# Kernel tuning notes

Measured on AMD Instinct MI355X. Metric: run time of the kernel, lower is better.

## Reference

```python
import jax, jax.numpy as jnp
import numpy as np

HEADS = 8
DIM_HEAD = 64
SCALE = DIM_HEAD ** -0.5


def setup_inputs() -> dict:
    key = jax.random.key(0)
    k1, k2, k3 = jax.random.split(key, 3)
    B, N, D = 4, 2048, HEADS * DIM_HEAD  # D = inner_dim = 512
    x = jax.random.normal(k1, (B, N, D), dtype=jnp.float32)
    # nn.Linear weights stored transposed vs torch; here we use [in, out]
    w_qkv = jax.random.normal(k2, (D, 3 * D), dtype=jnp.float32) * (D ** -0.5)
    w_out = jax.random.normal(k3, (D, D), dtype=jnp.float32) * (D ** -0.5)
    b_out = jnp.zeros((D,), dtype=jnp.float32)
    return {"x": x, "w_qkv": w_qkv, "w_out": w_out, "b_out": b_out}


def reference(x, w_qkv, w_out, b_out):
    B, N, D = x.shape
    qkv = x @ w_qkv  # [B, N, 3D]
    q, k, v = jnp.split(qkv, 3, axis=-1)

    def to_heads(t):  # b n (h d) -> b h n d
        return t.reshape(B, N, HEADS, DIM_HEAD).transpose(0, 2, 1, 3)

    q, k, v = to_heads(q), to_heads(k), to_heads(v)
    dots = jnp.einsum('bhnd,bhmd->bhnm', q, k) * SCALE  # [B,H,N,N]
    attn = jax.nn.softmax(dots, axis=-1)
    out = jnp.einsum('bhnm,bhmd->bhnd', attn, v)  # [B,H,N,d]
    out = out.transpose(0, 2, 1, 3).reshape(B, N, D)  # b h n d -> b n (h d)
    return out @ w_out + b_out
```

## Files before the change

### kernel.cpp

```cpp
#include <hip/hip_runtime.h>

typedef __bf16 bf16;
typedef __bf16 bf16x8 __attribute__((ext_vector_type(8)));
typedef __bf16 bf16x4 __attribute__((ext_vector_type(4)));
typedef float f32x4 __attribute__((ext_vector_type(4)));
typedef float f32x16 __attribute__((ext_vector_type(16)));

#define MFMA16(a, b, c) __builtin_amdgcn_mfma_f32_16x16x32_bf16(a, b, c, 0, 0, 0)
#define MFMA32(a, b, c) __builtin_amdgcn_mfma_f32_32x32x16_bf16(a, b, c, 0, 0, 0)

#define CS 0.18033688011112042f

#if __has_builtin(__builtin_amdgcn_exp2f)
#define EXP2(x) __builtin_amdgcn_exp2f(x)
#else
#define EXP2(x) exp2f(x)
#endif

#define WAIT_VM0() __builtin_amdgcn_s_waitcnt(0x0F70)

__device__ __forceinline__ void load_lds16(const bf16* g, bf16* l) {
    __builtin_amdgcn_global_load_lds(
        (const __attribute__((address_space(1))) unsigned int*)g,
        (__attribute__((address_space(3))) unsigned int*)l, 16, 0, 0);
}

__device__ __forceinline__ bf16x4 shfl_xor32_b64(bf16x4 v) {
    union { bf16x4 b; int i[2]; } u;
    u.b = v;
    u.i[0] = __shfl_xor(u.i[0], 32, 64);
    u.i[1] = __shfl_xor(u.i[1], 32, 64);
    return u.b;
}

__device__ __forceinline__ bf16x8 build_bfrag(bf16x4 plo, bf16x4 phi, int h) {
    bf16x4 xlo = shfl_xor32_b64(plo);
    bf16x4 xhi = shfl_xor32_b64(phi);
    bf16x4 lo4 = h ? xhi : plo;
    bf16x4 hi4 = h ? phi : xlo;
    bf16x8 bb;
#pragma unroll
    for (int i = 0; i < 4; ++i) { bb[i] = lo4[i]; bb[4 + i] = hi4[i]; }
    return bb;
}

__global__ __launch_bounds__(256) void f32_to_bf16_kernel(const float* __restrict__ in,
                                                          bf16* __restrict__ out, int n) {
    int i = (blockIdx.x * 256 + threadIdx.x) * 4;
    if (i < n) {
        float4 v = *(const float4*)&in[i];
        bf16x4 o = {(bf16)v.x, (bf16)v.y, (bf16)v.z, (bf16)v.w};
        *(bf16x4*)&out[i] = o;
    }
}

__global__ __launch_bounds__(256) void transpose_f2b(const float* __restrict__ in,
                                                     bf16* __restrict__ out,
                                                     int R, int C) {
    __shared__ float tile[32][33];
    int tx = threadIdx.x & 31, ty = threadIdx.x >> 5;
    int c0 = blockIdx.x * 32, r0 = blockIdx.y * 32;
#pragma unroll
    for (int i = ty; i < 32; i += 8)
        tile[i][tx] = in[(size_t)(r0 + i) * C + c0 + tx];
    __syncthreads();
#pragma unroll
    for (int i = ty; i < 32; i += 8)
        out[(size_t)(c0 + i) * R + r0 + tx] = (bf16)tile[tx][i];
}

__global__ __launch_bounds__(256) void transpose_v_kernel(const bf16* __restrict__ qkv,
                                                          bf16* __restrict__ vt) {
    __shared__ bf16 tile[32][33];
    int tx = threadIdx.x & 31, ty = threadIdx.x >> 5;
    int bh = blockIdx.z, b = bh >> 3, h = bh & 7;
    int n0 = blockIdx.x * 32, d0 = blockIdx.y * 32;
#pragma unroll
    for (int i = ty; i < 32; i += 8)
        tile[i][tx] = qkv[(size_t)(b * 2048 + n0 + i) * 1536 + 1024 + h * 64 + d0 + tx];
    __syncthreads();
#pragma unroll
    for (int i = ty; i < 32; i += 8)
        vt[(size_t)(bh * 64 + d0 + i) * 2048 + n0 + tx] = tile[tx][i];
}

template <int MT, int MODE, typename OutT>
__global__ __launch_bounds__(256, (MT == 4) ? 2 : 4)
void gemm_bt_kernel(const bf16* __restrict__ A,
                    const bf16* __restrict__ Bt,
                    const float* __restrict__ bias,
                    OutT* __restrict__ C,
                    int M, int N, int K) {
    const int BM = MT * 32;
    __shared__ bf16 As[BM * 64];
    __shared__ bf16 Bs[128 * 64];
    int t = threadIdx.x;
    int lane = t & 63, w = t >> 6;
    int wr = w >> 1, wc = w & 1;
    int quad = lane >> 4, r16 = lane & 15;
    int m0 = blockIdx.y * BM, n0 = blockIdx.x * 128;

    const f32x4 fzero = {0.f, 0.f, 0.f, 0.f};
    f32x4 acc[MT][4];
#pragma unroll
    for (int i = 0; i < MT; ++i)
#pragma unroll
        for (int j = 0; j < 4; ++j) acc[i][j] = fzero;

    const bf16* ap[MT]; bf16* ad[MT];
    const bf16* bp[4];  bf16* bd[4];
#pragma unroll
    for (int i = 0; i < MT; ++i) {
        int ci = i * 256 + t;
        int row = ci >> 3, cp = ci & 7, cc = cp ^ (row & 7);
        ap[i] = &A[(size_t)(m0 + row) * K + cc * 8];
        ad[i] = &As[ci * 8];
    }
#pragma unroll
    for (int i = 0; i < 4; ++i) {
        int ci = i * 256 + t;
        int row = ci >> 3, cp = ci & 7, cc = cp ^ (row & 7);
        bp[i] = &Bt[(size_t)(n0 + row) * K + cc * 8];
        bd[i] = &Bs[ci * 8];
    }

    for (int k0 = 0; k0 < K; k0 += 64) {
        __syncthreads();
#pragma unroll
        for (int i = 0; i < MT; ++i) { load_lds16(ap[i], ad[i]); ap[i] += 64; }
#pragma unroll
        for (int i = 0; i < 4; ++i) { load_lds16(bp[i], bd[i]); bp[i] += 64; }
        __syncthreads();
#pragma unroll
        for (int ks = 0; ks < 2; ++ks) {
            bf16x8 af[MT], bfr[4];
            int cp = (ks * 4 + quad) ^ (r16 & 7);
#pragma unroll
            for (int mt = 0; mt < MT; ++mt)
                af[mt] = *(const bf16x8*)&As[(wr * (BM / 2) + mt * 16 + r16) * 64 + cp * 8];
#pragma unroll
            for (int nt = 0; nt < 4; ++nt)
                bfr[nt] = *(const bf16x8*)&Bs[(wc * 64 + nt * 16 + r16) * 64 + cp * 8];
#pragma unroll
            for (int mt = 0; mt < MT; ++mt)
#pragma unroll
                for (int nt = 0; nt < 4; ++nt)
                    acc[mt][nt] = MFMA16(af[mt], bfr[nt], acc[mt][nt]);
        }
    }
#pragma unroll
    for (int mt = 0; mt < MT; ++mt)
#pragma unroll
        for (int nt = 0; nt < 4; ++nt)
#pragma unroll
            for (int r = 0; r < 4; ++r) {
                int row = m0 + wr * (BM / 2) + mt * 16 + quad * 4 + r;
                int col = n0 + wc * 64 + nt * 16 + r16;
                float v = acc[mt][nt][r];
                if (MODE == 1 && n0 < 512) v *= CS;
                if (MODE == 2) v += bias[col];
                C[(size_t)row * N + col] = (OutT)v;
            }
}

__global__ __launch_bounds__(128, 2) void attn_kernel(const bf16* __restrict__ qkv,
                                                      const bf16* __restrict__ vt,
                                                      bf16* __restrict__ out) {
    __shared__ __align__(16) char smemraw[18432];
    bf16* stage = (bf16*)smemraw;

    int t = threadIdx.x;
    int lane = t & 63, w = t >> 6;
    int h = lane >> 5, q = lane & 31;
    int bh = blockIdx.y, b = bh >> 3, hd = bh & 7;
    int qb = blockIdx.x * 64;

    bf16x8 qf[2][4];
#pragma unroll
    for (int sub = 0; sub < 2; ++sub) {
        size_t qoff = (size_t)(b * 2048 + qb + sub * 32 + q) * 1536 + hd * 64;
#pragma unroll
        for (int s = 0; s < 4; ++s)
            qf[sub][s] = *(const bf16x8*)&qkv[qoff + s * 16 + h * 8];
    }

    f32x16 o_acc[2][2];
#pragma unroll
    for (int sub = 0; sub < 2; ++sub)
#pragma unroll
        for (int db = 0; db < 2; ++db)
#pragma unroll
            for (int i = 0; i < 16; ++i) o_acc[sub][db][i] = 0.f;
    float psum[2] = {0.f, 0.f};

    bf16* Ks = stage + w * 4096;
    bf16* Vs = Ks + 2048;

    const bf16* kp[4]; const bf16* vp[4];
    bf16* kd[4]; bf16* vd[4];
#pragma unroll
    for (int rdd = 0; rdd < 4; ++rdd) {
        int ciK = rdd * 64 + lane;
        int rowK = ciK >> 3, ccK = (ciK & 7) ^ (rowK & 7);
        kp[rdd] = &qkv[(size_t)(b * 2048 + w * 1024 + rowK) * 1536 + 512 + hd * 64 + ccK * 8];
        kd[rdd] = &Ks[ciK * 8];
        int ciV = rdd * 64 + lane;
        int rowV = ciV >> 2, ccV = (ciV & 3) ^ (rowV & 3);
        vp[rdd] = &vt[(size_t)(bh * 64 + rowV) * 2048 + w * 1024 + ccV * 8];
        vd[rdd] = &Vs[ciV * 8];
    }

    for (int it = 0; it < 32; ++it) {
#pragma unroll
        for (int rdd = 0; rdd < 4; ++rdd) {
            load_lds16(kp[rdd], kd[rdd]); kp[rdd] += (size_t)32 * 1536;
            load_lds16(vp[rdd], vd[rdd]); vp[rdd] += 32;
        }
        WAIT_VM0();

        bf16x8 kf[4];
#pragma unroll
        for (int s = 0; s < 4; ++s) {
            int cp = (s * 2 + h) ^ (q & 7);
            kf[s] = *(const bf16x8*)&Ks[q * 64 + cp * 8];
        }
        bf16x8 vf[2][2];
#pragma unroll
        for (int kstep = 0; kstep < 2; ++kstep)
#pragma unroll
            for (int db = 0; db < 2; ++db) {
                int cp = (kstep * 2 + h) ^ (q & 3);
                vf[kstep][db] = *(const bf16x8*)&Vs[(db * 32 + q) * 32 + cp * 8];
            }

#pragma unroll
        for (int sub = 0; sub < 2; ++sub) {
            f32x16 sacc;
#pragma unroll
            for (int i = 0; i < 16; ++i) sacc[i] = 0.f;
#pragma unroll
            for (int s = 0; s < 4; ++s)
                sacc = MFMA32(kf[s], qf[sub][s], sacc);

            bf16x4 pk[4];
            float ps = 0.f;
#pragma unroll
            for (int g8 = 0; g8 < 4; ++g8)
#pragma unroll
                for (int i = 0; i < 4; ++i) {
                    float p = EXP2(sacc[4 * g8 + i]);
                    ps += p;
                    pk[g8][i] = (bf16)p;
                }
            psum[sub] += ps;
            bf16x8 bfr0 = build_bfrag(pk[0], pk[1], h);
            bf16x8 bfr1 = build_bfrag(pk[2], pk[3], h);

#pragma unroll
            for (int db = 0; db < 2; ++db) {
                o_acc[sub][db] = MFMA32(vf[0][db], bfr0, o_acc[sub][db]);
                o_acc[sub][db] = MFMA32(vf[1][db], bfr1, o_acc[sub][db]);
            }
        }
    }

    float l_own[2];
#pragma unroll
    for (int sub = 0; sub < 2; ++sub)
        l_own[sub] = psum[sub] + __shfl_xor(psum[sub], 32, 64);

    __syncthreads();
    float* Of = (float*)smemraw;
    float* Lf = (float*)(smemraw + 17408);

    if (w == 1) {
#pragma unroll
        for (int sub = 0; sub < 2; ++sub) {
#pragma unroll
            for (int db = 0; db < 2; ++db)
#pragma unroll
                for (int r = 0; r < 16; ++r) {
                    int d = db * 32 + (r & 3) + 8 * (r >> 2) + 4 * h;
                    Of[(sub * 32 + q) * 68 + d] = o_acc[sub][db][r];
                }
            if (h == 0) Lf[sub * 32 + q] = l_own[sub];
        }
    }
    __syncthreads();
    if (w == 0) {
#pragma unroll
        for (int sub = 0; sub < 2; ++sub) {
#pragma unroll
            for (int db = 0; db < 2; ++db)
#pragma unroll
                for (int r = 0; r < 16; ++r) {
                    int d = db * 32 + (r & 3) + 8 * (r >> 2) + 4 * h;
                    Of[(sub * 32 + q) * 68 + d] += o_acc[sub][db][r];
                }
            if (h == 0) Lf[sub * 32 + q] += l_own[sub];
        }
    }
    __syncthreads();

    {
        int row = t >> 1, half = t & 1;
        float linv = 1.f / Lf[row];
        const float* src = &Of[row * 68 + half * 32];
        bf16* dst = &out[(size_t)(b * 2048 + qb + row) * 512 + hd * 64 + half * 32];
#pragma unroll
        for (int i = 0; i < 4; ++i) {
            f32x4 a = *(const f32x4*)&src[i * 8];
            f32x4 c = *(const f32x4*)&src[i * 8 + 4];
            bf16x8 o8;
#pragma unroll
            for (int j = 0; j < 4; ++j) {
                o8[j] = (bf16)(a[j] * linv);
                o8[4 + j] = (bf16)(c[j] * linv);
            }
            *(bf16x8*)&dst[i * 8] = o8;
        }
    }
}

extern "C" void kernel_launch(void* const* d_in, const int* in_sizes, int n_in,
                              void* d_out, int out_size, void* d_ws, size_t ws_size,
                              hipStream_t stream) {
    const float* x     = (const float*)d_in[0];
    const float* w_qkv = (const float*)d_in[1];
    const float* w_out = (const float*)d_in[2];
    const float* b_out = (const float*)d_in[3];
    float* out = (float*)d_out;

    char* ws = (char*)d_ws;
    size_t off = 0;
    bf16* xb    = (bf16*)(ws + off); off += (size_t)8192 * 512 * 2;
    bf16* wqkvT = (bf16*)(ws + off); off += (size_t)1536 * 512 * 2;
    bf16* woutT = (bf16*)(ws + off); off += (size_t)512 * 512 * 2;
    bf16* qkv   = (bf16*)(ws + off); off += (size_t)8192 * 1536 * 2;
    bf16* vt    = (bf16*)(ws + off); off += (size_t)32 * 64 * 2048 * 2;
    bf16* attn  = (bf16*)(ws + off);

    f32_to_bf16_kernel<<<4096, 256, 0, stream>>>(x, xb, 8192 * 512);
    transpose_f2b<<<dim3(48, 16), 256, 0, stream>>>(w_qkv, wqkvT, 512, 1536);
    transpose_f2b<<<dim3(16, 16), 256, 0, stream>>>(w_out, woutT, 512, 512);
    gemm_bt_kernel<4, 1, bf16><<<dim3(12, 64), 256, 0, stream>>>(
        xb, wqkvT, nullptr, qkv, 8192, 1536, 512);
    transpose_v_kernel<<<dim3(64, 2, 32), 256, 0, stream>>>(qkv, vt);
    attn_kernel<<<dim3(32, 32), 128, 0, stream>>>(qkv, vt, attn);
    gemm_bt_kernel<2, 2, float><<<dim3(4, 128), 256, 0, stream>>>(
        attn, woutT, b_out, out, 8192, 512, 512);
}
```

Baseline: 170.9 us.

## Split attention KV range across four waves and load K/V directly to registers

```diff
diff --git a/kernel.cpp b/kernel.cpp
--- a/kernel.cpp
+++ b/kernel.cpp
@@ -16,8 +16,6 @@
 #else
 #define EXP2(x) exp2f(x)
 #endif
-
-#define WAIT_VM0() __builtin_amdgcn_s_waitcnt(0x0F70)
 
 __device__ __forceinline__ void load_lds16(const bf16* g, bf16* l) {
     __builtin_amdgcn_global_load_lds(
@@ -163,11 +161,10 @@
             }
 }
 
-__global__ __launch_bounds__(128, 2) void attn_kernel(const bf16* __restrict__ qkv,
+__global__ __launch_bounds__(256, 4) void attn_kernel(const bf16* __restrict__ qkv,
                                                       const bf16* __restrict__ vt,
                                                       bf16* __restrict__ out) {
-    __shared__ __align__(16) char smemraw[18432];
-    bf16* stage = (bf16*)smemraw;
+    __shared__ __align__(16) char smemraw[35328];
 
     int t = threadIdx.x;
     int lane = t & 63, w = t >> 6;
@@ -193,45 +190,23 @@
             for (int i = 0; i < 16; ++i) o_acc[sub][db][i] = 0.f;
     float psum[2] = {0.f, 0.f};
 
-    bf16* Ks = stage + w * 4096;
-    bf16* Vs = Ks + 2048;
-
-    const bf16* kp[4]; const bf16* vp[4];
-    bf16* kd[4]; bf16* vd[4];
-#pragma unroll
-    for (int rdd = 0; rdd < 4; ++rdd) {
-        int ciK = rdd * 64 + lane;
-        int rowK = ciK >> 3, ccK = (ciK & 7) ^ (rowK & 7);
-        kp[rdd] = &qkv[(size_t)(b * 2048 + w * 1024 + rowK) * 1536 + 512 + hd * 64 + ccK * 8];
-        kd[rdd] = &Ks[ciK * 8];
-        int ciV = rdd * 64 + lane;
-        int rowV = ciV >> 2, ccV = (ciV & 3) ^ (rowV & 3);
-        vp[rdd] = &vt[(size_t)(bh * 64 + rowV) * 2048 + w * 1024 + ccV * 8];
-        vd[rdd] = &Vs[ciV * 8];
-    }
-
-    for (int it = 0; it < 32; ++it) {
-#pragma unroll
-        for (int rdd = 0; rdd < 4; ++rdd) {
-            load_lds16(kp[rdd], kd[rdd]); kp[rdd] += (size_t)32 * 1536;
-            load_lds16(vp[rdd], vd[rdd]); vp[rdd] += 32;
-        }
-        WAIT_VM0();
-
-        bf16x8 kf[4];
-#pragma unroll
-        for (int s = 0; s < 4; ++s) {
-            int cp = (s * 2 + h) ^ (q & 7);
-            kf[s] = *(const bf16x8*)&Ks[q * 64 + cp * 8];
-        }
-        bf16x8 vf[2][2];
-#pragma unroll
-        for (int kstep = 0; kstep < 2; ++kstep)
-#pragma unroll
-            for (int db = 0; db < 2; ++db) {
-                int cp = (kstep * 2 + h) ^ (q & 3);
-                vf[kstep][db] = *(const bf16x8*)&Vs[(db * 32 + q) * 32 + cp * 8];
-            }
+    const bf16* kp = &qkv[(size_t)(b * 2048 + w * 512 + q) * 1536 + 512 + hd * 64 + h * 8];
+    const bf16* vp0 = &vt[(size_t)(bh * 64 + q) * 2048 + w * 512 + h * 8];
+    const bf16* vp1 = vp0 + (size_t)32 * 2048;
+
+    for (int it = 0; it < 16; ++it) {
+        bf16x8 kf[4], vf[2][2];
+#pragma unroll
+        for (int s = 0; s < 4; ++s)
+            kf[s] = *(const bf16x8*)&kp[s * 16];
+#pragma unroll
+        for (int kstep = 0; kstep < 2; ++kstep) {
+            vf[kstep][0] = *(const bf16x8*)&vp0[kstep * 16];
+            vf[kstep][1] = *(const bf16x8*)&vp1[kstep * 16];
+        }
+        kp += (size_t)32 * 1536;
+        vp0 += 32;
+        vp1 += 32;
 
 #pragma unroll
         for (int sub = 0; sub < 2; ++sub) {
@@ -269,11 +244,14 @@
     for (int sub = 0; sub < 2; ++sub)
         l_own[sub] = psum[sub] + __shfl_xor(psum[sub], 32, 64);
 
-    __syncthreads();
     float* Of = (float*)smemraw;
-    float* Lf = (float*)(smemraw + 17408);
-
-    if (w == 1) {
+    float* Lf = (float*)(smemraw + 34816);
+    int slab = w & 1;
+    float* myOf = Of + slab * 64 * 68;
+    float* myLf = Lf + slab * 64;
+
+    __syncthreads();
+    if (w >= 2) {
 #pragma unroll
         for (int sub = 0; sub < 2; ++sub) {
 #pragma unroll
@@ -281,13 +259,13 @@
 #pragma unroll
                 for (int r = 0; r < 16; ++r) {
                     int d = db * 32 + (r & 3) + 8 * (r >> 2) + 4 * h;
-                    Of[(sub * 32 + q) * 68 + d] = o_acc[sub][db][r];
+                    myOf[(sub * 32 + q) * 68 + d] = o_acc[sub][db][r];
                 }
-            if (h == 0) Lf[sub * 32 + q] = l_own[sub];
-        }
-    }
-    __syncthreads();
-    if (w == 0) {
+            if (h == 0) myLf[sub * 32 + q] = l_own[sub];
+        }
+    }
+    __syncthreads();
+    if (w < 2) {
 #pragma unroll
         for (int sub = 0; sub < 2; ++sub) {
 #pragma unroll
@@ -295,29 +273,26 @@
 #pragma unroll
                 for (int r = 0; r < 16; ++r) {
                     int d = db * 32 + (r & 3) + 8 * (r >> 2) + 4 * h;
-                    Of[(sub * 32 + q) * 68 + d] += o_acc[sub][db][r];
+                    myOf[(sub * 32 + q) * 68 + d] += o_acc[sub][db][r];
                 }
-            if (h == 0) Lf[sub * 32 + q] += l_own[sub];
+            if (h == 0) myLf[sub * 32 + q] += l_own[sub];
         }
     }
     __syncthreads();
 
     {
-        int row = t >> 1, half = t & 1;
-        float linv = 1.f / Lf[row];
-        const float* src = &Of[row * 68 + half * 32];
-        bf16* dst = &out[(size_t)(b * 2048 + qb + row) * 512 + hd * 64 + half * 32];
-#pragma unroll
-        for (int i = 0; i < 4; ++i) {
-            f32x4 a = *(const f32x4*)&src[i * 8];
-            f32x4 c = *(const f32x4*)&src[i * 8 + 4];
+        int row = t >> 2, seg = t & 3;
+        float linv = 1.f / (Lf[row] + Lf[64 + row]);
+        const float* s0 = &Of[row * 68 + seg * 16];
+        const float* s1 = &Of[64 * 68 + row * 68 + seg * 16];
+        bf16* dst = &out[(size_t)(b * 2048 + qb + row) * 512 + hd * 64 + seg * 16];
+#pragma unroll
+        for (int half = 0; half < 2; ++half) {
             bf16x8 o8;
 #pragma unroll
-            for (int j = 0; j < 4; ++j) {
-                o8[j] = (bf16)(a[j] * linv);
-                o8[4 + j] = (bf16)(c[j] * linv);
-            }
-            *(bf16x8*)&dst[i * 8] = o8;
+            for (int j = 0; j < 8; ++j)
+                o8[j] = (bf16)((s0[half * 8 + j] + s1[half * 8 + j]) * linv);
+            *(bf16x8*)&dst[half * 8] = o8;
         }
     }
 }
@@ -346,7 +321,7 @@
     gemm_bt_kernel<4, 1, bf16><<<dim3(12, 64), 256, 0, stream>>>(
         xb, wqkvT, nullptr, qkv, 8192, 1536, 512);
     transpose_v_kernel<<<dim3(64, 2, 32), 256, 0, stream>>>(qkv, vt);
-    attn_kernel<<<dim3(32, 32), 128, 0, stream>>>(qkv, vt, attn);
+    attn_kernel<<<dim3(32, 32), 256, 0, stream>>>(qkv, vt, attn);
     gemm_bt_kernel<2, 2, float><<<dim3(4, 128), 256, 0, stream>>>(
         attn, woutT, b_out, out, 8192, 512, 512);
 }
```

Result: slower. 296.8 us (+73.7%).
